# Performance work log

Hardware: AMD Instinct MI355X
Metric: run time of the kernel (lower is better)

The kernel has to match this reference:

```python
import jax, jax.numpy as jnp
import numpy as np

C = 256

def setup_inputs() -> dict:
    key = jax.random.key(0)
    ks = jax.random.split(key, 7)
    s = 1.0 / np.sqrt(C)
    x = jax.random.normal(ks[0], (4, C, 64, 64), dtype=jnp.float32)
    Wq = jax.random.uniform(ks[1], (C, C), jnp.float32, -s, s)
    bq = jax.random.uniform(ks[2], (C,), jnp.float32, -s, s)
    Wk = jax.random.uniform(ks[3], (C, C), jnp.float32, -s, s)
    bk = jax.random.uniform(ks[4], (C,), jnp.float32, -s, s)
    Wv = jax.random.uniform(ks[5], (C, C), jnp.float32, -s, s)
    bv = jax.random.uniform(ks[6], (C,), jnp.float32, -s, s)
    return {"x": x, "Wq": Wq, "bq": bq, "Wk": Wk, "bk": bk, "Wv": Wv, "bv": bv}

def reference(x, Wq, bq, Wk, bk, Wv, bv):
    B, Cc, H, W = x.shape
    N = H * W
    xf = x.reshape(B, Cc, N)                      # (B, C, N)
    # 1x1 conv == channel linear: out[b,o,n] = sum_c W[o,c] x[b,c,n] + b[o]
    q = jnp.einsum('oc,bcn->bno', Wq, xf) + bq    # (B, N, C)  proj_query^T
    k = jnp.einsum('oc,bcn->bon', Wk, xf) + bk[None, :, None]  # (B, C, N)
    v = jnp.einsum('oc,bcn->bon', Wv, xf) + bv[None, :, None]  # (B, C, N)
    energy = jnp.einsum('bnc,bcm->bnm', q, k)     # (B, N, N)
    attention = jax.nn.softmax(energy, axis=-1)
    # out = V @ attention^T : out[b,c,n] = sum_m v[b,c,m] * attention[b,n,m]
    out = jnp.einsum('bcm,bnm->bcn', v, attention)
    return out.reshape(B, Cc, H, W)
```

## Files before the change

### kernel.cpp

```cpp
#include <hip/hip_runtime.h>
#include <math.h>

#define BB 4
#define CC 256
#define NN 4096
#define KV 64

using half8 = __attribute__((ext_vector_type(8))) _Float16;
using f32x4 = __attribute__((ext_vector_type(4))) float;
using f32x16 = __attribute__((ext_vector_type(16))) float;

__device__ __forceinline__ unsigned short f2h(float f) {
  _Float16 h = (_Float16)f;
  return __builtin_bit_cast(unsigned short, h);
}
__device__ __forceinline__ float h2f(unsigned short u) {
  return (float)__builtin_bit_cast(_Float16, u);
}
__device__ __forceinline__ unsigned int pk2(float a, float b) {
  __attribute__((ext_vector_type(2))) __fp16 h = __builtin_amdgcn_cvt_pkrtz(a, b);
  return __builtin_bit_cast(unsigned int, h);
}

#define ASYNC16(g, l)                                                        \
  __builtin_amdgcn_global_load_lds(                                          \
      (const __attribute__((address_space(1))) unsigned int*)(g),            \
      (__attribute__((address_space(3))) unsigned int*)(l), 16, 0, 0)

__device__ __forceinline__ int vt_off(int r, int chunk) {
  return r * 64 + (((chunk ^ r) & 7) << 3);
}

__global__ __launch_bounds__(256) void k_wcast(const float* __restrict__ Wq,
    const float* __restrict__ Wk, const float* __restrict__ Wv,
    unsigned short* __restrict__ Wt) {
  int id = blockIdx.x * 256 + threadIdx.x;
  int pos8 = id & 7, o = (id >> 3) & 255, ks = (id >> 11) & 3, p3 = id >> 13;
  const float* W = p3 == 0 ? Wq : (p3 == 1 ? Wk : Wv);
  int c = ks * 64 + ((pos8 ^ o) & 7) * 8;
  const float* src = W + (size_t)o * CC + c;
  float4 a = *(const float4*)(src);
  float4 b4 = *(const float4*)(src + 4);
  union { unsigned short u[8]; uint4 v4; } pk;
  pk.u[0] = f2h(a.x);  pk.u[1] = f2h(a.y);  pk.u[2] = f2h(a.z);  pk.u[3] = f2h(a.w);
  pk.u[4] = f2h(b4.x); pk.u[5] = f2h(b4.y); pk.u[6] = f2h(b4.z); pk.u[7] = f2h(b4.w);
  *(uint4*)(Wt + (size_t)id * 8) = pk.v4;
}

__global__ __launch_bounds__(512) void k_proj(const float* __restrict__ x,
    const unsigned short* __restrict__ Wt,
    const float* __restrict__ bq, const float* __restrict__ bk,
    const float* __restrict__ bv,
    unsigned short* __restrict__ Q, unsigned short* __restrict__ K,
    unsigned short* __restrict__ V) {
  __shared__ __align__(16) char ps[110848];
  float* xf = (float*)ps;
  unsigned short* xa = (unsigned short*)(ps + 8448);
  unsigned short* wh = (unsigned short*)(ps + 12544);
  int b = blockIdx.y, n0 = blockIdx.x * 32;
  int t = threadIdx.x, w = t >> 6, lane = t & 63, l15 = lane & 15, quad = lane >> 4;

  f32x4 z = {0.f, 0.f, 0.f, 0.f};
  f32x4 acc[3][2][2];
#pragma unroll
  for (int p3 = 0; p3 < 3; ++p3)
#pragma unroll
    for (int ct = 0; ct < 2; ++ct)
#pragma unroll
      for (int mt = 0; mt < 2; ++mt) acc[p3][ct][mt] = z;

  for (int ks = 0; ks < 4; ++ks) {
    if (ks) __syncthreads();
#pragma unroll
    for (int p3 = 0; p3 < 3; ++p3) {
      const char* wb = (const char*)(Wt + (size_t)(p3 * 4 + ks) * 16384);
#pragma unroll
      for (int p = 0; p < 4; ++p) {
        int c = p * 512 + t;
        ASYNC16(wb + c * 16, &wh[p3 * 16384 + (p * 512 + (w << 6)) * 8]);
      }
    }
    {
      int c = t >> 3, nl = (t & 7) * 4;
      float4 v = *(const float4*)(x + ((size_t)b * CC + ks * 64 + c) * NN + n0 + nl);
      float* d = xf + c * 33 + nl;
      d[0] = v.x; d[1] = v.y; d[2] = v.z; d[3] = v.w;
    }
    __syncthreads();
    {
      int n = t >> 4, cb = (t & 15) * 4;
      union { unsigned short u[4]; ushort4 v4; } tmp;
#pragma unroll
      for (int i = 0; i < 4; ++i) tmp.u[i] = f2h(xf[(cb + i) * 33 + n]);
      int ch = cb >> 3;
      *(ushort4*)&xa[n * 64 + (((ch ^ n) & 7) << 3) + (cb & 7)] = tmp.v4;
    }
    __syncthreads();
#pragma unroll
    for (int kc = 0; kc < 2; ++kc) {
      half8 af[2];
#pragma unroll
      for (int mt = 0; mt < 2; ++mt)
        af[mt] = *(const half8*)&xa[vt_off(mt * 16 + l15, kc * 4 + quad)];
#pragma unroll
      for (int p3 = 0; p3 < 3; ++p3)
#pragma unroll
        for (int ct = 0; ct < 2; ++ct) {
          half8 bf = *(const half8*)&wh[p3 * 16384 + vt_off(w * 32 + ct * 16 + l15, kc * 4 + quad)];
#pragma unroll
          for (int mt = 0; mt < 2; ++mt)
            acc[p3][ct][mt] = __builtin_amdgcn_mfma_f32_16x16x32_f16(af[mt], bf, acc[p3][ct][mt], 0, 0, 0);
        }
    }
  }
#pragma unroll
  for (int p3 = 0; p3 < 3; ++p3) {
    const float* bias = p3 == 0 ? bq : (p3 == 1 ? bk : bv);
#pragma unroll
    for (int ct = 0; ct < 2; ++ct) {
      float bv_ = bias[w * 32 + ct * 16 + l15];
#pragma unroll
      for (int mt = 0; mt < 2; ++mt)
#pragma unroll
        for (int r = 0; r < 4; ++r) acc[p3][ct][mt][r] += bv_;
    }
  }
#pragma unroll
  for (int p3 = 0; p3 < 2; ++p3) {
    __syncthreads();
    unsigned short* qo = (unsigned short*)ps;
#pragma unroll
    for (int ct = 0; ct < 2; ++ct)
#pragma unroll
      for (int mt = 0; mt < 2; ++mt)
#pragma unroll
        for (int r = 0; r < 4; ++r)
          qo[(mt * 16 + quad * 4 + r) * 264 + w * 32 + ct * 16 + l15] = f2h(acc[p3][ct][mt][r]);
    __syncthreads();
    unsigned short* outp = (p3 == 0 ? Q : K) + ((size_t)b * NN + n0) * CC;
#pragma unroll
    for (int p = 0; p < 2; ++p) {
      int f = p * 8192 + t * 16;
      int n = f >> 9, off = f & 511;
      *(uint4*)((char*)outp + (size_t)n * 512 + off) =
        *(const uint4*)((const char*)&qo[n * 264] + off);
    }
  }
  {
    __syncthreads();
    unsigned short* vo = (unsigned short*)ps;
#pragma unroll
    for (int ct = 0; ct < 2; ++ct)
#pragma unroll
      for (int mt = 0; mt < 2; ++mt)
#pragma unroll
        for (int r = 0; r < 4; ++r)
          vo[(w * 32 + ct * 16 + l15) * 36 + mt * 16 + quad * 4 + r] = f2h(acc[2][ct][mt][r]);
    __syncthreads();
#pragma unroll
    for (int p = 0; p < 2; ++p) {
      int id = p * 512 + t;
      int o = id >> 2, off = (id & 3) * 16;
      *(uint4*)((char*)(V + ((size_t)b * CC + o) * NN + n0) + off) =
        *(const uint4*)((const char*)&vo[o * 36] + off);
    }
  }
}

__global__ __launch_bounds__(512, 2) void k_flash(const unsigned short* __restrict__ Q,
    const unsigned short* __restrict__ K, const unsigned short* __restrict__ V,
    float* __restrict__ out, unsigned short* __restrict__ opart,
    float* __restrict__ ml, int n_splits) {
  __shared__ __align__(16) char sm[133120];
  unsigned short* kt0 = (unsigned short*)sm;
  unsigned short* kt1 = (unsigned short*)(sm + 32768);
  unsigned short* vt0 = (unsigned short*)(sm + 65536);
  unsigned short* vt1 = (unsigned short*)(sm + 98304);
  float* mm_ = (float*)(sm + 131072);
  float* ll_ = (float*)(sm + 132096);

  int b = blockIdx.y, q0 = blockIdx.x * 128, split = blockIdx.z;
  int nt = (NN / KV) / n_splits;
  int t = threadIdx.x, w = t >> 6, lane = t & 63;
  int qn = lane & 31, hi = lane >> 5;
  int qg = w >> 1, kth = w & 1;

  half8 qf[16];
  {
    const unsigned short* qrow = Q + ((size_t)b * NN + q0 + qg * 32 + qn) * CC;
#pragma unroll
    for (int cs = 0; cs < 16; ++cs)
      qf[cs] = *(const half8*)(qrow + cs * 16 + hi * 8);
  }

  f32x16 o_acc[8];
#pragma unroll
  for (int ct = 0; ct < 8; ++ct)
#pragma unroll
    for (int r = 0; r < 16; ++r) o_acc[ct][r] = 0.f;

  float m_i = -INFINITY, lp = 0.f;

  int it_beg = split * nt, it_end = it_beg + nt;

  auto dma_k = [&](int it, unsigned short* dst) {
    const char* kb = (const char*)(K + ((size_t)b * NN + it * KV) * CC);
#pragma unroll
    for (int p = 0; p < 4; ++p) {
      int c = p * 512 + t;
      int r = c >> 5, chp = c & 31;
      ASYNC16(kb + r * 512 + ((chp ^ (r & 31)) << 4), &dst[(p * 512 + (w << 6)) * 8]);
    }
  };
  auto dma_v = [&](int it, unsigned short* dst) {
    const char* vb = (const char*)(V + (size_t)b * CC * NN) + it * 128;
#pragma unroll
    for (int p = 0; p < 4; ++p) {
      int c = p * 512 + t;
      int r = c >> 3, chp = c & 7;
      ASYNC16(vb + (size_t)r * 8192 + ((chp ^ (r & 7)) << 4), &dst[(p * 512 + (w << 6)) * 8]);
    }
  };

  dma_k(it_beg, (it_beg & 1) ? kt1 : kt0);
  dma_v(it_beg, (it_beg & 1) ? vt1 : vt0);

  for (int it = it_beg; it < it_end; ++it) {
    int par = it & 1;
    const unsigned short* kcur = par ? kt1 : kt0;
    const unsigned short* vcur = par ? vt1 : vt0;

    asm volatile("s_waitcnt vmcnt(4)" ::: "memory");
    __builtin_amdgcn_s_barrier();
    __builtin_amdgcn_sched_barrier(0);

    if (it + 1 < it_end) {
      dma_k(it + 1, par ? kt0 : kt1);
      dma_v(it + 1, par ? vt0 : vt1);
    }

    f32x16 sa;
#pragma unroll
    for (int r = 0; r < 16; ++r) sa[r] = 0.f;
    __builtin_amdgcn_s_setprio(1);
#pragma unroll
    for (int cs = 0; cs < 16; ++cs) {
      half8 kf = *(const half8*)&kcur[(kth * 32 + qn) * 256 + ((((cs * 2 + hi) ^ qn) & 31) << 3)];
      sa = __builtin_amdgcn_mfma_f32_32x32x16_f16(kf, qf[cs], sa, 0, 0, 0);
    }
    __builtin_amdgcn_s_setprio(0);

    float pm = sa[0];
#pragma unroll
    for (int r = 1; r < 16; ++r) pm = fmaxf(pm, sa[r]);
    pm = fmaxf(pm, __shfl_xor(pm, 32, 64));
    if (!__all(pm <= m_i + 8.0f)) {
      float mnew = fmaxf(m_i, pm);
      float alpha = __expf(m_i - mnew);
      m_i = mnew;
      lp *= alpha;
#pragma unroll
      for (int ct = 0; ct < 8; ++ct)
#pragma unroll
        for (int r = 0; r < 16; ++r) o_acc[ct][r] *= alpha;
    }
    float ls = 0.f;
#pragma unroll
    for (int r = 0; r < 16; ++r) {
      float p = __expf(sa[r] - m_i);
      sa[r] = p;
      ls += p;
    }
    lp += ls;

    unsigned int g0x = pk2(sa[0],  sa[1]);
    unsigned int g0y = pk2(sa[2],  sa[3]);
    unsigned int g1x = pk2(sa[4],  sa[5]);
    unsigned int g1y = pk2(sa[6],  sa[7]);
    unsigned int g2x = pk2(sa[8],  sa[9]);
    unsigned int g2y = pk2(sa[10], sa[11]);
    unsigned int g3x = pk2(sa[12], sa[13]);
    unsigned int g3y = pk2(sa[14], sa[15]);

    if (it + 1 < it_end) {
      asm volatile("s_waitcnt vmcnt(8)" ::: "memory");
    } else {
      asm volatile("s_waitcnt vmcnt(0)" ::: "memory");
    }
    __builtin_amdgcn_s_barrier();
    __builtin_amdgcn_sched_barrier(0);

    __builtin_amdgcn_s_setprio(1);
#pragma unroll
    for (int s = 0; s < 2; ++s) {
      unsigned int ax = s ? g2x : g0x, ay = s ? g2y : g0y;
      unsigned int bx = s ? g3x : g1x, by = s ? g3y : g1y;
      unsigned int vx = hi ? ax : bx, vy = hi ? ay : by;
      unsigned int xx = (unsigned int)__shfl_xor((int)vx, 32, 64);
      unsigned int xy = (unsigned int)__shfl_xor((int)vy, 32, 64);
      union { unsigned int u[4]; half8 h; } bf;
      bf.u[0] = hi ? xx : ax;
      bf.u[1] = hi ? xy : ay;
      bf.u[2] = hi ? bx : xx;
      bf.u[3] = hi ? by : xy;
#pragma unroll
      for (int ct = 0; ct < 8; ++ct) {
        half8 af = *(const half8*)&vcur[(ct * 32 + qn) * 64 + ((((kth * 4 + s * 2 + hi) ^ (qn & 7)) & 7) << 3)];
        o_acc[ct] = __builtin_amdgcn_mfma_f32_32x32x16_f16(af, bf.h, o_acc[ct], 0, 0, 0);
      }
    }
    __builtin_amdgcn_s_setprio(0);
  }

  lp += __shfl_xor(lp, 32, 64);
  if (lane < 32) {
    mm_[kth * 128 + qg * 32 + lane] = m_i;
    ll_[kth * 128 + qg * 32 + lane] = lp;
  }
  __syncthreads();
  float m_oth = mm_[(kth ^ 1) * 128 + qg * 32 + qn];
  float l_oth = ll_[(kth ^ 1) * 128 + qg * 32 + qn];
  float M = fmaxf(m_i, m_oth);
  float myw = __expf(m_i - M);
  float lcomb = lp * myw + l_oth * __expf(m_oth - M);

  float* od0 = (float*)sm;
  float* od1 = od0 + 32 * 132;
  float* linv = (float*)(sm + 33792);
  if (kth == 0 && lane < 32) {
    int q = qg * 32 + lane;
    linv[q] = 1.0f / lcomb;
    if (n_splits != 1) {
      size_t qi = (size_t)q0 + q;
      ml[((size_t)(split * 2 + 0) * BB + b) * NN + qi] = M;
      ml[((size_t)(split * 2 + 1) * BB + b) * NN + qi] = lcomb;
    }
  }
  __syncthreads();

  float* obf = out + (size_t)b * CC * NN + q0;
  unsigned short* obh = opart + ((size_t)split * BB + b) * CC * NN + q0;
#pragma unroll
  for (int ct = 0; ct < 8; ++ct) {
    float* od = kth ? od1 : od0;
#pragma unroll
    for (int r = 0; r < 16; ++r) {
      int cl = (r & 3) + 8 * (r >> 2) + 4 * hi;
      od[cl * 132 + qg * 32 + qn] = o_acc[ct][r] * myw;
    }
    __syncthreads();
    {
      int row = t >> 4, q8 = (t & 15) * 8;
      f32x4 a0 = *(const f32x4*)&od0[row * 132 + q8];
      f32x4 a1 = *(const f32x4*)&od0[row * 132 + q8 + 4];
      f32x4 b0 = *(const f32x4*)&od1[row * 132 + q8];
      f32x4 b1 = *(const f32x4*)&od1[row * 132 + q8 + 4];
      f32x4 l0 = *(const f32x4*)&linv[q8];
      f32x4 l1 = *(const f32x4*)&linv[q8 + 4];
      f32x4 s0, s1;
#pragma unroll
      for (int i = 0; i < 4; ++i) {
        s0[i] = (a0[i] + b0[i]) * l0[i];
        s1[i] = (a1[i] + b1[i]) * l1[i];
      }
      if (n_splits == 1) {
        *(f32x4*)(obf + (size_t)(ct * 32 + row) * NN + q8) = s0;
        *(f32x4*)(obf + (size_t)(ct * 32 + row) * NN + q8 + 4) = s1;
      } else {
        union { unsigned short u[8]; uint4 v4; } tmp;
#pragma unroll
        for (int i = 0; i < 4; ++i) { tmp.u[i] = f2h(s0[i]); tmp.u[4 + i] = f2h(s1[i]); }
        *(uint4*)(obh + (size_t)(ct * 32 + row) * NN + q8) = tmp.v4;
      }
    }
    __syncthreads();
  }
}

__global__ __launch_bounds__(256) void k_merge(const unsigned short* __restrict__ opart,
    const float* __restrict__ ml, float* __restrict__ out) {
  size_t i = ((size_t)blockIdx.x * 256 + threadIdx.x) * 4;
  int n = (int)(i & (NN - 1));
  int b = (int)(i >> 20);
  float4 m1 = *(const float4*)(ml + ((size_t)(0 * BB) + b) * NN + n);
  float4 l1 = *(const float4*)(ml + ((size_t)(1 * BB) + b) * NN + n);
  float4 m2 = *(const float4*)(ml + ((size_t)(2 * BB) + b) * NN + n);
  float4 l2 = *(const float4*)(ml + ((size_t)(3 * BB) + b) * NN + n);
  ushort4 o1 = *(const ushort4*)(opart + i);
  ushort4 o2 = *(const ushort4*)(opart + (size_t)BB * CC * NN + i);
  float4 res;
#define MRG(f, comp) { \
    float M = fmaxf(m1.f, m2.f); \
    float e1 = __expf(m1.f - M) * l1.f, e2 = __expf(m2.f - M) * l2.f; \
    res.f = (e1 * h2f(o1.comp) + e2 * h2f(o2.comp)) / (e1 + e2); }
  MRG(x, x) MRG(y, y) MRG(z, z) MRG(w, w)
#undef MRG
  *(float4*)(out + i) = res;
}

extern "C" void kernel_launch(void* const* d_in, const int* in_sizes, int n_in,
                              void* d_out, int out_size, void* d_ws, size_t ws_size,
                              hipStream_t stream) {
  const float* x  = (const float*)d_in[0];
  const float* Wq = (const float*)d_in[1];
  const float* bq = (const float*)d_in[2];
  const float* Wk = (const float*)d_in[3];
  const float* bk = (const float*)d_in[4];
  const float* Wv = (const float*)d_in[5];
  const float* bv = (const float*)d_in[6];
  float* out = (float*)d_out;
  char* ws = (char*)d_ws;
  const size_t MB = 1024 * 1024;
  unsigned short* Qb = (unsigned short*)(ws);
  unsigned short* Kb = (unsigned short*)(ws + 8 * MB);
  unsigned short* Vb = (unsigned short*)(ws + 16 * MB);
  unsigned short* Op = (unsigned short*)(ws + 24 * MB);
  float*          Ml = (float*)(ws + 40 * MB);

  int ns = (ws_size >= 41 * MB) ? 2 : 1;
  unsigned short* Wt = (unsigned short*)(ns == 2 ? ws + 40 * MB + 256 * 1024
                                                 : ws + 24 * MB);

  k_wcast<<<dim3(96), 256, 0, stream>>>(Wq, Wk, Wv, Wt);
  k_proj<<<dim3(128, 4), 512, 0, stream>>>(x, Wt, bq, bk, bv, Qb, Kb, Vb);

  k_flash<<<dim3(32, 4, ns), 512, 0, stream>>>(Qb, Kb, Vb, out, Op, Ml, ns);
  if (ns == 2) k_merge<<<dim3(4096), 256, 0, stream>>>(Op, Ml, out);
}
```

Baseline: 224.9 us.

## Software-pipeline PV of previous tile with QK of current tile in flash loop

Restructures the flash-attention loop so the P·V MFMAs for the previous KV tile are interleaved with the Q·K MFMAs of the current tile, with a triple-buffered V tile in LDS and the packed probabilities carried across iterations. This drops the second barrier and wait inside each iteration, leaving one synchronisation point per tile, and lets the exp/softmax work overlap with matrix work. In exchange, LDS use grows to 160KB, which may restrict blocks per CU, and the loop now waits on all outstanding loads (vmcnt(0)) at the top of each iteration.

```diff
diff --git a/kernel.cpp b/kernel.cpp
--- a/kernel.cpp
+++ b/kernel.cpp
@@ -171,13 +171,9 @@
     const unsigned short* __restrict__ K, const unsigned short* __restrict__ V,
     float* __restrict__ out, unsigned short* __restrict__ opart,
     float* __restrict__ ml, int n_splits) {
-  __shared__ __align__(16) char sm[133120];
+  __shared__ __align__(16) char sm[163840];
   unsigned short* kt0 = (unsigned short*)sm;
   unsigned short* kt1 = (unsigned short*)(sm + 32768);
-  unsigned short* vt0 = (unsigned short*)(sm + 65536);
-  unsigned short* vt1 = (unsigned short*)(sm + 98304);
-  float* mm_ = (float*)(sm + 131072);
-  float* ll_ = (float*)(sm + 132096);
 
   int b = blockIdx.y, q0 = blockIdx.x * 128, split = blockIdx.z;
   int nt = (NN / KV) / n_splits;
@@ -200,9 +196,13 @@
     for (int r = 0; r < 16; ++r) o_acc[ct][r] = 0.f;
 
   float m_i = -INFINITY, lp = 0.f;
+  half8 bfp0, bfp1;
 
   int it_beg = split * nt, it_end = it_beg + nt;
 
+  auto vtb = [&](int i) -> unsigned short* {
+    return (unsigned short*)(sm + 65536 + i * 32768);
+  };
   auto dma_k = [&](int it, unsigned short* dst) {
     const char* kb = (const char*)(K + ((size_t)b * NN + it * KV) * CC);
 #pragma unroll
@@ -222,31 +222,43 @@
     }
   };
 
+  int vcur = it_beg % 3;
   dma_k(it_beg, (it_beg & 1) ? kt1 : kt0);
-  dma_v(it_beg, (it_beg & 1) ? vt1 : vt0);
+  dma_v(it_beg, vtb(vcur));
 
   for (int it = it_beg; it < it_end; ++it) {
     int par = it & 1;
     const unsigned short* kcur = par ? kt1 : kt0;
-    const unsigned short* vcur = par ? vt1 : vt0;
-
-    asm volatile("s_waitcnt vmcnt(4)" ::: "memory");
+    const unsigned short* vprev = vtb((vcur + 2) % 3);
+
+    asm volatile("s_waitcnt vmcnt(0)" ::: "memory");
     __builtin_amdgcn_s_barrier();
     __builtin_amdgcn_sched_barrier(0);
 
     if (it + 1 < it_end) {
       dma_k(it + 1, par ? kt0 : kt1);
-      dma_v(it + 1, par ? vt0 : vt1);
+      dma_v(it + 1, vtb((vcur + 1) % 3));
     }
 
     f32x16 sa;
 #pragma unroll
     for (int r = 0; r < 16; ++r) sa[r] = 0.f;
     __builtin_amdgcn_s_setprio(1);
-#pragma unroll
-    for (int cs = 0; cs < 16; ++cs) {
-      half8 kf = *(const half8*)&kcur[(kth * 32 + qn) * 256 + ((((cs * 2 + hi) ^ qn) & 31) << 3)];
-      sa = __builtin_amdgcn_mfma_f32_32x32x16_f16(kf, qf[cs], sa, 0, 0, 0);
+    if (it > it_beg) {
+#pragma unroll
+      for (int cs = 0; cs < 16; ++cs) {
+        half8 kf = *(const half8*)&kcur[(kth * 32 + qn) * 256 + ((((cs * 2 + hi) ^ qn) & 31) << 3)];
+        sa = __builtin_amdgcn_mfma_f32_32x32x16_f16(kf, qf[cs], sa, 0, 0, 0);
+        int ct = cs & 7, s = cs >> 3;
+        half8 af = *(const half8*)&vprev[(ct * 32 + qn) * 64 + ((((kth * 4 + s * 2 + hi) ^ (qn & 7)) & 7) << 3)];
+        o_acc[ct] = __builtin_amdgcn_mfma_f32_32x32x16_f16(af, s ? bfp1 : bfp0, o_acc[ct], 0, 0, 0);
+      }
+    } else {
+#pragma unroll
+      for (int cs = 0; cs < 16; ++cs) {
+        half8 kf = *(const half8*)&kcur[(kth * 32 + qn) * 256 + ((((cs * 2 + hi) ^ qn) & 31) << 3)];
+        sa = __builtin_amdgcn_mfma_f32_32x32x16_f16(kf, qf[cs], sa, 0, 0, 0);
+      }
     }
     __builtin_amdgcn_s_setprio(0);
 
@@ -282,15 +294,6 @@
     unsigned int g3x = pk2(sa[12], sa[13]);
     unsigned int g3y = pk2(sa[14], sa[15]);
 
-    if (it + 1 < it_end) {
-      asm volatile("s_waitcnt vmcnt(8)" ::: "memory");
-    } else {
-      asm volatile("s_waitcnt vmcnt(0)" ::: "memory");
-    }
-    __builtin_amdgcn_s_barrier();
-    __builtin_amdgcn_sched_barrier(0);
-
-    __builtin_amdgcn_s_setprio(1);
 #pragma unroll
     for (int s = 0; s < 2; ++s) {
       unsigned int ax = s ? g2x : g0x, ay = s ? g2y : g0y;
@@ -303,16 +306,29 @@
       bf.u[1] = hi ? xy : ay;
       bf.u[2] = hi ? bx : xx;
       bf.u[3] = hi ? by : xy;
+      if (s) bfp1 = bf.h; else bfp0 = bf.h;
+    }
+
+    vcur = (vcur + 1) % 3;
+  }
+
+  {
+    const unsigned short* vlast = vtb((vcur + 2) % 3);
+    __builtin_amdgcn_s_setprio(1);
+#pragma unroll
+    for (int s = 0; s < 2; ++s)
 #pragma unroll
       for (int ct = 0; ct < 8; ++ct) {
-        half8 af = *(const half8*)&vcur[(ct * 32 + qn) * 64 + ((((kth * 4 + s * 2 + hi) ^ (qn & 7)) & 7) << 3)];
-        o_acc[ct] = __builtin_amdgcn_mfma_f32_32x32x16_f16(af, bf.h, o_acc[ct], 0, 0, 0);
-      }
-    }
+        half8 af = *(const half8*)&vlast[(ct * 32 + qn) * 64 + ((((kth * 4 + s * 2 + hi) ^ (qn & 7)) & 7) << 3)];
+        o_acc[ct] = __builtin_amdgcn_mfma_f32_32x32x16_f16(af, s ? bfp1 : bfp0, o_acc[ct], 0, 0, 0);
+      }
     __builtin_amdgcn_s_setprio(0);
   }
 
+  float* mm_ = (float*)(sm + 65536);
+  float* ll_ = (float*)(sm + 65536 + 1024);
   lp += __shfl_xor(lp, 32, 64);
+  __syncthreads();
   if (lane < 32) {
     mm_[kth * 128 + qg * 32 + lane] = m_i;
     ll_[kth * 128 + qg * 32 + lane] = lp;
```

Result: slower. 273.7 us (+21.7%).

## Remap split blocks, simplify barriers, and split QK MFMA chain into two accumulators

Applied to the files above, without the earlier changes.

When there are two splits, the flash kernel now remaps block indices so that blocks sharing a batch and split are interleaved, aiming for better L2 reuse of K/V. It replaces the two partial vmcnt waits with their barriers by a single __syncthreads at the top of each iteration. It also splits the QK^T MFMA chain into two independent accumulators that are summed afterwards, to shorten the dependency chain. The single full wait removes the overlap of V-tile loading with the QK phase, which may expose more memory latency.

```diff
diff --git a/kernel.cpp b/kernel.cpp
--- a/kernel.cpp
+++ b/kernel.cpp
@@ -179,7 +179,16 @@
   float* mm_ = (float*)(sm + 131072);
   float* ll_ = (float*)(sm + 132096);
 
-  int b = blockIdx.y, q0 = blockIdx.x * 128, split = blockIdx.z;
+  int b, q0, split;
+  if (n_splits == 2) {
+    int lin = blockIdx.x + 32 * (blockIdx.y + 4 * blockIdx.z);
+    int g = lin & 7;
+    b = g & 3;
+    split = g >> 2;
+    q0 = (lin >> 3) * 128;
+  } else {
+    b = blockIdx.y; split = blockIdx.z; q0 = blockIdx.x * 128;
+  }
   int nt = (NN / KV) / n_splits;
   int t = threadIdx.x, w = t >> 6, lane = t & 63;
   int qn = lane & 31, hi = lane >> 5;
@@ -230,25 +239,28 @@
     const unsigned short* kcur = par ? kt1 : kt0;
     const unsigned short* vcur = par ? vt1 : vt0;
 
-    asm volatile("s_waitcnt vmcnt(4)" ::: "memory");
-    __builtin_amdgcn_s_barrier();
-    __builtin_amdgcn_sched_barrier(0);
+    __syncthreads();
 
     if (it + 1 < it_end) {
       dma_k(it + 1, par ? kt0 : kt1);
       dma_v(it + 1, par ? vt0 : vt1);
     }
 
+    f32x16 sa0, sa1;
+#pragma unroll
+    for (int r = 0; r < 16; ++r) { sa0[r] = 0.f; sa1[r] = 0.f; }
+    __builtin_amdgcn_s_setprio(1);
+#pragma unroll
+    for (int cs = 0; cs < 16; cs += 2) {
+      half8 kf0 = *(const half8*)&kcur[(kth * 32 + qn) * 256 + ((((cs * 2 + hi) ^ qn) & 31) << 3)];
+      half8 kf1 = *(const half8*)&kcur[(kth * 32 + qn) * 256 + (((((cs + 1) * 2 + hi) ^ qn) & 31) << 3)];
+      sa0 = __builtin_amdgcn_mfma_f32_32x32x16_f16(kf0, qf[cs], sa0, 0, 0, 0);
+      sa1 = __builtin_amdgcn_mfma_f32_32x32x16_f16(kf1, qf[cs + 1], sa1, 0, 0, 0);
+    }
+    __builtin_amdgcn_s_setprio(0);
     f32x16 sa;
 #pragma unroll
-    for (int r = 0; r < 16; ++r) sa[r] = 0.f;
-    __builtin_amdgcn_s_setprio(1);
-#pragma unroll
-    for (int cs = 0; cs < 16; ++cs) {
-      half8 kf = *(const half8*)&kcur[(kth * 32 + qn) * 256 + ((((cs * 2 + hi) ^ qn) & 31) << 3)];
-      sa = __builtin_amdgcn_mfma_f32_32x32x16_f16(kf, qf[cs], sa, 0, 0, 0);
-    }
-    __builtin_amdgcn_s_setprio(0);
+    for (int r = 0; r < 16; ++r) sa[r] = sa0[r] + sa1[r];
 
     float pm = sa[0];
 #pragma unroll
@@ -281,14 +293,6 @@
     unsigned int g2y = pk2(sa[10], sa[11]);
     unsigned int g3x = pk2(sa[12], sa[13]);
     unsigned int g3y = pk2(sa[14], sa[15]);
-
-    if (it + 1 < it_end) {
-      asm volatile("s_waitcnt vmcnt(8)" ::: "memory");
-    } else {
-      asm volatile("s_waitcnt vmcnt(0)" ::: "memory");
-    }
-    __builtin_amdgcn_s_barrier();
-    __builtin_amdgcn_sched_barrier(0);
 
     __builtin_amdgcn_s_setprio(1);
 #pragma unroll
```

Result: slower. 248.1 us (+10.3%).
